# Kernel tuning notes

Hardware: AMD Instinct MI355X
Metric: run time of the kernel (lower is better)

## Reference

```python
import jax, jax.numpy as jnp
import numpy as np

BATCH, IN_F, OUT_F = 8192, 2048, 2048
LN2 = float(np.log(2.0))


def setup_inputs() -> dict:
    key = jax.random.key(0)
    kx, kw = jax.random.split(key)
    x = jax.random.normal(kx, (BATCH, IN_F), dtype=jnp.float32)
    # kaiming_uniform_(a=sqrt(5)) on (OUT_F, IN_F+1): U(-1/sqrt(fan_in), 1/sqrt(fan_in))
    bound = 1.0 / np.sqrt(IN_F + 1)
    W = jax.random.uniform(kw, (OUT_F, IN_F + 1), dtype=jnp.float32,
                           minval=-bound, maxval=bound)
    W = W.at[:, -1].set(0.0)  # bias column initialized to 0
    return {"x": x, "W": W}


def reference(x, W):
    # UniversalKANNode forward, node_type='add', use_bias=True,
    # function = lshifted_softplus: f(x, w) = w * (softplus(x) - ln2)
    # Append bias ones column: (B, IN_F+1)
    xb = jnp.concatenate([x, jnp.ones((x.shape[0], 1), dtype=x.dtype)], axis=-1)
    phi = jax.nn.softplus(xb) - jnp.asarray(LN2, dtype=x.dtype)  # (B, IN_F+1)
    # sum over input dim of W[o,i] * phi[b,i]  ==  GEMM
    return jnp.einsum("bi,oi->bo", phi, W)  # (B, OUT_F)
```

## Files before the change

### kernel.cpp

```cpp
#include <hip/hip_runtime.h>

#define M_DIM 8192
#define N_DIM 2048
#define K_DIM 2048
#define LN2F 0.69314718055994530942f
#define LOG2EF 1.44269504088896340736f
#define BIAS_PHI 0.62009741f

typedef _Float16 f16x8 __attribute__((ext_vector_type(8)));
typedef float f32x4 __attribute__((ext_vector_type(4)));

__device__ __forceinline__ float softplus_m_ln2(float v) {
    float t = v * LOG2EF;
    float e = __builtin_amdgcn_exp2f(t);
    float r = (__builtin_amdgcn_logf(1.0f + e) - 1.0f) * LN2F;
    return t < 24.0f ? r : v - LN2F;
}

__global__ __launch_bounds__(256) void prep_kernel(const float* __restrict__ x,
                                                   const float* __restrict__ W,
                                                   _Float16* __restrict__ phi,
                                                   _Float16* __restrict__ Wh,
                                                   float* __restrict__ bias) {
    if (blockIdx.x < 8192) {
        size_t i = ((size_t)blockIdx.x * blockDim.x + threadIdx.x) * 8;
        float4 v0 = *(const float4*)(x + i);
        float4 v1 = *(const float4*)(x + i + 4);
        union { _Float16 h[8]; uint4 u; } pk;
        pk.h[0] = (_Float16)softplus_m_ln2(v0.x);
        pk.h[1] = (_Float16)softplus_m_ln2(v0.y);
        pk.h[2] = (_Float16)softplus_m_ln2(v0.z);
        pk.h[3] = (_Float16)softplus_m_ln2(v0.w);
        pk.h[4] = (_Float16)softplus_m_ln2(v1.x);
        pk.h[5] = (_Float16)softplus_m_ln2(v1.y);
        pk.h[6] = (_Float16)softplus_m_ln2(v1.z);
        pk.h[7] = (_Float16)softplus_m_ln2(v1.w);
        *(uint4*)(phi + i) = pk.u;
    } else {
        const int o = blockIdx.x - 8192;
        const float* row = W + (size_t)o * (K_DIM + 1) + threadIdx.x * 8;
        union { _Float16 h[8]; uint4 u; } pk;
#pragma unroll
        for (int j = 0; j < 8; ++j)
            pk.h[j] = (_Float16)row[j];
        *(uint4*)(Wh + (size_t)o * K_DIM + threadIdx.x * 8) = pk.u;
        if (threadIdx.x == 0)
            bias[o] = W[(size_t)o * (K_DIM + 1) + K_DIM] * BIAS_PHI;
    }
}

__global__ __launch_bounds__(256, 2) void kan_gemm(const _Float16* __restrict__ A,
                                                   const _Float16* __restrict__ B,
                                                   const float* __restrict__ bias,
                                                   float* __restrict__ C) {
    __shared__ __align__(16) _Float16 sA[256 * 64];
    __shared__ __align__(16) _Float16 sB[128 * 64];

    const int tid  = threadIdx.x;
    const int lane = tid & 63;
    const int wv   = tid >> 6;

    const size_t Arow0 = (size_t)blockIdx.x * 256;
    const size_t Brow0 = (size_t)blockIdx.y * 128;

    const int r8 = lane >> 3;
    const int lc = (lane & 7) ^ r8;

    const _Float16* gA = A + (Arow0 + wv * 64 + r8) * (size_t)K_DIM + lc * 8;
    _Float16* sAw = &sA[wv * 64 * 64];
    const _Float16* gB = B + (Brow0 + wv * 32 + r8) * (size_t)K_DIM + lc * 8;
    _Float16* sBw = &sB[wv * 32 * 64];

    const int wr = (wv >> 1) * 128;
    const int wc = (wv & 1) * 64;
    const int lr   = lane & 15;
    const int kph0 = ((lane >> 4) ^ (lr & 7)) * 8;

    f32x4 acc[8][4];
#pragma unroll
    for (int i = 0; i < 8; ++i)
#pragma unroll
        for (int j = 0; j < 4; ++j)
            acc[i][j] = (f32x4){0.0f, 0.0f, 0.0f, 0.0f};

    for (int k0 = 0; k0 < K_DIM; k0 += 64) {
        __syncthreads();
#pragma unroll
        for (int j = 0; j < 8; ++j)
            __builtin_amdgcn_global_load_lds(
                (const __attribute__((address_space(1))) void*)(gA + k0 + (size_t)j * 8 * K_DIM),
                (__attribute__((address_space(3))) void*)(sAw + j * 8 * 64), 16, 0, 0);
#pragma unroll
        for (int j = 0; j < 4; ++j)
            __builtin_amdgcn_global_load_lds(
                (const __attribute__((address_space(1))) void*)(gB + k0 + (size_t)j * 8 * K_DIM),
                (__attribute__((address_space(3))) void*)(sBw + j * 8 * 64), 16, 0, 0);
        __syncthreads();

#pragma unroll
        for (int kc = 0; kc < 2; ++kc) {
            const int ko = kph0 ^ (kc * 32);
            f16x8 bfr[4];
#pragma unroll
            for (int ni = 0; ni < 4; ++ni)
                bfr[ni] = *(const f16x8*)&sB[(wc + ni * 16 + lr) * 64 + ko];

#pragma unroll
            for (int mh = 0; mh < 2; ++mh) {
                f16x8 af[4];
#pragma unroll
                for (int mi = 0; mi < 4; ++mi)
                    af[mi] = *(const f16x8*)&sA[(wr + (mh * 4 + mi) * 16 + lr) * 64 + ko];
#pragma unroll
                for (int mi = 0; mi < 4; ++mi)
#pragma unroll
                    for (int ni = 0; ni < 4; ++ni)
                        acc[mh * 4 + mi][ni] = __builtin_amdgcn_mfma_f32_16x16x32_f16(
                            af[mi], bfr[ni], acc[mh * 4 + mi][ni], 0, 0, 0);
            }
        }
    }

    const int crow = (lane >> 4) * 4;
    float bsv[4];
#pragma unroll
    for (int ni = 0; ni < 4; ++ni)
        bsv[ni] = bias[Brow0 + wc + ni * 16 + lr];

#pragma unroll
    for (int mi = 0; mi < 8; ++mi) {
#pragma unroll
        for (int r = 0; r < 4; ++r) {
            float* cp = C + (Arow0 + wr + mi * 16 + crow + r) * (size_t)N_DIM
                        + Brow0 + wc + lr;
#pragma unroll
            for (int ni = 0; ni < 4; ++ni)
                cp[ni * 16] = acc[mi][ni][r] + bsv[ni];
        }
    }
}

extern "C" void kernel_launch(void* const* d_in, const int* in_sizes, int n_in,
                              void* d_out, int out_size, void* d_ws, size_t ws_size,
                              hipStream_t stream) {
    const float* x = (const float*)d_in[0];
    const float* W = (const float*)d_in[1];
    float* out = (float*)d_out;

    char* ws = (char*)d_ws;
    _Float16* phi = (_Float16*)ws;
    _Float16* Wh  = (_Float16*)(ws + (size_t)M_DIM * K_DIM * sizeof(_Float16));
    float* bias   = (float*)(ws + (size_t)M_DIM * K_DIM * sizeof(_Float16)
                                + (size_t)N_DIM * K_DIM * sizeof(_Float16));

    prep_kernel<<<8192 + 2048, 256, 0, stream>>>(x, W, phi, Wh, bias);
    dim3 grid(M_DIM / 256, N_DIM / 128);
    kan_gemm<<<grid, 256, 0, stream>>>(phi, Wh, bias, out);
}
```

Measured before the change: 185.0 us.

## Double-buffer LDS tiles with K=32 stages to overlap global loads with MFMA

```diff
diff --git a/kernel.cpp b/kernel.cpp
--- a/kernel.cpp
+++ b/kernel.cpp
@@ -6,6 +6,9 @@
 #define LN2F 0.69314718055994530942f
 #define LOG2EF 1.44269504088896340736f
 #define BIAS_PHI 0.62009741f
+
+#define WAIT_VM6 0x0F76
+#define WAIT_VM0 0x0F70
 
 typedef _Float16 f16x8 __attribute__((ext_vector_type(8)));
 typedef float f32x4 __attribute__((ext_vector_type(4)));
@@ -53,8 +56,8 @@
                                                    const _Float16* __restrict__ B,
                                                    const float* __restrict__ bias,
                                                    float* __restrict__ C) {
-    __shared__ __align__(16) _Float16 sA[256 * 64];
-    __shared__ __align__(16) _Float16 sB[128 * 64];
+    __shared__ __align__(16) _Float16 sA[2][256 * 32];
+    __shared__ __align__(16) _Float16 sB[2][128 * 32];
 
     const int tid  = threadIdx.x;
     const int lane = tid & 63;
@@ -63,18 +66,16 @@
     const size_t Arow0 = (size_t)blockIdx.x * 256;
     const size_t Brow0 = (size_t)blockIdx.y * 128;
 
-    const int r8 = lane >> 3;
-    const int lc = (lane & 7) ^ r8;
+    const int rS = lane >> 2;
+    const int cS = ((lane & 3) ^ ((lane >> 3) & 3)) * 8;
 
-    const _Float16* gA = A + (Arow0 + wv * 64 + r8) * (size_t)K_DIM + lc * 8;
-    _Float16* sAw = &sA[wv * 64 * 64];
-    const _Float16* gB = B + (Brow0 + wv * 32 + r8) * (size_t)K_DIM + lc * 8;
-    _Float16* sBw = &sB[wv * 32 * 64];
+    const _Float16* gA = A + (Arow0 + wv * 64 + rS) * (size_t)K_DIM + cS;
+    const _Float16* gB = B + (Brow0 + wv * 32 + rS) * (size_t)K_DIM + cS;
 
     const int wr = (wv >> 1) * 128;
     const int wc = (wv & 1) * 64;
-    const int lr   = lane & 15;
-    const int kph0 = ((lane >> 4) ^ (lr & 7)) * 8;
+    const int lr  = lane & 15;
+    const int kqs = ((lane >> 4) ^ ((lr >> 1) & 3)) * 8;
 
     f32x4 acc[8][4];
 #pragma unroll
@@ -83,41 +84,55 @@
         for (int j = 0; j < 4; ++j)
             acc[i][j] = (f32x4){0.0f, 0.0f, 0.0f, 0.0f};
 
-    for (int k0 = 0; k0 < K_DIM; k0 += 64) {
-        __syncthreads();
-#pragma unroll
-        for (int j = 0; j < 8; ++j)
-            __builtin_amdgcn_global_load_lds(
-                (const __attribute__((address_space(1))) void*)(gA + k0 + (size_t)j * 8 * K_DIM),
-                (__attribute__((address_space(3))) void*)(sAw + j * 8 * 64), 16, 0, 0);
+    auto stage = [&](int k0, int buf) {
+        const _Float16* ga = gA + k0;
+        const _Float16* gb = gB + k0;
+        _Float16* da = &sA[buf][wv * 64 * 32];
+        _Float16* db = &sB[buf][wv * 32 * 32];
 #pragma unroll
         for (int j = 0; j < 4; ++j)
             __builtin_amdgcn_global_load_lds(
-                (const __attribute__((address_space(1))) void*)(gB + k0 + (size_t)j * 8 * K_DIM),
-                (__attribute__((address_space(3))) void*)(sBw + j * 8 * 64), 16, 0, 0);
-        __syncthreads();
+                (const __attribute__((address_space(1))) void*)(ga + (size_t)j * 16 * K_DIM),
+                (__attribute__((address_space(3))) void*)(da + j * 16 * 32), 16, 0, 0);
+#pragma unroll
+        for (int j = 0; j < 2; ++j)
+            __builtin_amdgcn_global_load_lds(
+                (const __attribute__((address_space(1))) void*)(gb + (size_t)j * 16 * K_DIM),
+                (__attribute__((address_space(3))) void*)(db + j * 16 * 32), 16, 0, 0);
+    };
+
+    stage(0, 0);
+
+    for (int k = 0; k < 64; ++k) {
+        const int p = k & 1;
+        __builtin_amdgcn_s_barrier();
+        if (k < 63) {
+            stage((k + 1) * 32, 1 - p);
+            __builtin_amdgcn_s_waitcnt(WAIT_VM6);
+        } else {
+            __builtin_amdgcn_s_waitcnt(WAIT_VM0);
+        }
+        __builtin_amdgcn_s_barrier();
+
+        const _Float16* sAp = sA[p];
+        const _Float16* sBp = sB[p];
+        f16x8 bfr[4];
+#pragma unroll
+        for (int ni = 0; ni < 4; ++ni)
+            bfr[ni] = *(const f16x8*)&sBp[(wc + ni * 16 + lr) * 32 + kqs];
 
 #pragma unroll
-        for (int kc = 0; kc < 2; ++kc) {
-            const int ko = kph0 ^ (kc * 32);
-            f16x8 bfr[4];
+        for (int mh = 0; mh < 2; ++mh) {
+            f16x8 af[4];
 #pragma unroll
-            for (int ni = 0; ni < 4; ++ni)
-                bfr[ni] = *(const f16x8*)&sB[(wc + ni * 16 + lr) * 64 + ko];
-
+            for (int mi = 0; mi < 4; ++mi)
+                af[mi] = *(const f16x8*)&sAp[(wr + (mh * 4 + mi) * 16 + lr) * 32 + kqs];
 #pragma unroll
-            for (int mh = 0; mh < 2; ++mh) {
-                f16x8 af[4];
+            for (int mi = 0; mi < 4; ++mi)
 #pragma unroll
-                for (int mi = 0; mi < 4; ++mi)
-                    af[mi] = *(const f16x8*)&sA[(wr + (mh * 4 + mi) * 16 + lr) * 64 + ko];
-#pragma unroll
-                for (int mi = 0; mi < 4; ++mi)
-#pragma unroll
-                    for (int ni = 0; ni < 4; ++ni)
-                        acc[mh * 4 + mi][ni] = __builtin_amdgcn_mfma_f32_16x16x32_f16(
-                            af[mi], bfr[ni], acc[mh * 4 + mi][ni], 0, 0, 0);
-            }
+                for (int ni = 0; ni < 4; ++ni)
+                    acc[mh * 4 + mi][ni] = __builtin_amdgcn_mfma_f32_16x16x32_f16(
+                        af[mi], bfr[ni], acc[mh * 4 + mi][ni], 0, 0, 0);
         }
     }
 
```

New measurement: 196.3 us. 6.1% more time.
